# Performance work log

Measured on AMD Instinct MI355X. Metric: run time of the kernel, lower is better.

The kernel has to match this reference:

```python
import jax, jax.numpy as jnp
import numpy as np

HEADS = 12
FEATURES = 768
D_HEAD = FEATURES // HEADS
SCALE = float(np.sqrt(D_HEAD))
EPS = 1e-12
N = 2048


def setup_inputs() -> dict:
    key = jax.random.key(0)
    ks = jax.random.split(key, 5)
    init = 1.0 / np.sqrt(FEATURES)
    return {
        "x": jax.random.normal(ks[0], (N, FEATURES), dtype=jnp.float32),
        "Wq": jax.random.normal(ks[1], (FEATURES, FEATURES), dtype=jnp.float32) * init,
        "Wk": jax.random.normal(ks[2], (FEATURES, FEATURES), dtype=jnp.float32) * init,
        "Wv": jax.random.normal(ks[3], (FEATURES, FEATURES), dtype=jnp.float32) * init,
        "Wo": jax.random.normal(ks[4], (FEATURES, FEATURES), dtype=jnp.float32) * init,
        "gamma": jnp.ones((FEATURES,), dtype=jnp.float32),
        "beta": jnp.zeros((FEATURES,), dtype=jnp.float32),
    }


def reference(x, Wq, Wk, Wv, Wo, gamma, beta):
    n = x.shape[0]
    # projections (no bias); weight layout [out, in] -> x @ W.T
    q = (x @ Wq.T).reshape(n, HEADS, D_HEAD).transpose(1, 0, 2)  # [h, n, d]
    k = (x @ Wk.T).reshape(n, HEADS, D_HEAD).transpose(1, 0, 2)
    v = (x @ Wv.T).reshape(n, HEADS, D_HEAD).transpose(1, 0, 2)
    # scores [h, n, n]; original divides q@k^T by sqrt(d_head)
    att = jnp.einsum("hnd,hmd->hnm", q, k) / SCALE
    att = jax.nn.softmax(att, axis=-1)  # dropout p=0 -> identity
    out = jnp.einsum("hnm,hmd->hnd", att, v)  # [h, n, d]
    out = out.transpose(1, 0, 2).reshape(n, FEATURES)  # n (h d)
    out = out @ Wo.T
    # residual + layernorm (eps=1e-12)
    y = out + x
    mu = jnp.mean(y, axis=-1, keepdims=True)
    var = jnp.mean((y - mu) ** 2, axis=-1, keepdims=True)
    return (y - mu) / jnp.sqrt(var + EPS) * gamma + beta
```

## Files before the change

### kernel.cpp

```cpp
#include <hip/hip_runtime.h>
#include <hip/hip_bf16.h>
#include <math.h>

#define N_TOK 2048
#define FEAT  768
#define HEADS 12
#define DHEAD 64
#define SPLIT 4
#define KV_PER (N_TOK / SPLIT)

typedef __bf16 v8bf __attribute__((ext_vector_type(8)));
typedef __bf16 v4bf __attribute__((ext_vector_type(4)));
typedef float  v4f  __attribute__((ext_vector_type(4)));

#define XE ((size_t)N_TOK * FEAT)
#define WE ((size_t)FEAT * FEAT)
#define QK_LD 1536

#define SCALE_FOLD 0.18033688011112042f

__device__ __forceinline__ void gload16(const __bf16* g, __bf16* l) {
    __builtin_amdgcn_global_load_lds(
        (const __attribute__((address_space(1))) unsigned int*)g,
        (__attribute__((address_space(3))) unsigned int*)l, 16, 0, 0);
}

__global__ __launch_bounds__(256) void cvt_all(
        const float* __restrict__ x,  const float* __restrict__ Wq,
        const float* __restrict__ Wk, const float* __restrict__ Wv,
        const float* __restrict__ Wo,
        __bf16* __restrict__ xb, __bf16* __restrict__ wqkv, __bf16* __restrict__ wob) {
    size_t i = ((size_t)blockIdx.x * 256 + threadIdx.x) * 4;
    const float* src; __bf16* dst; size_t off; float scale = 1.f;
    if (i < XE)               { src = x;  dst = xb;          off = i; }
    else if (i < XE + WE)     { src = Wq; dst = wqkv;        off = i - XE; scale = SCALE_FOLD; }
    else if (i < XE + 2 * WE) { src = Wk; dst = wqkv + WE;   off = i - XE - WE; }
    else if (i < XE + 3 * WE) { src = Wv; dst = wqkv + 2*WE; off = i - XE - 2*WE; }
    else                      { src = Wo; dst = wob;         off = i - XE - 3*WE; }
    float4 v = *(const float4*)(src + off);
    v4bf o;
    o[0] = (__bf16)(v.x * scale); o[1] = (__bf16)(v.y * scale);
    o[2] = (__bf16)(v.z * scale); o[3] = (__bf16)(v.w * scale);
    *(v4bf*)(dst + off) = o;
}

__global__ __launch_bounds__(256) void gemm_qkv(
        const __bf16* __restrict__ A, const __bf16* __restrict__ B,
        __bf16* __restrict__ qk, __bf16* __restrict__ vt) {
    __shared__ __bf16 As[64][32];
    __shared__ __bf16 Bs[128][32];
    const int t    = threadIdx.x;
    const int lane = t & 63, w = t >> 6;
    const int quad = lane >> 4, l15 = lane & 15;
    const int wm = w & 1, wn = w >> 1;
    const int bm = blockIdx.y * 64, bn = blockIdx.x * 128;
    const int srow = lane >> 2, scol = (lane & 3) * 8;

    v4f acc[2][4] = {};
    for (int k0 = 0; k0 < FEAT; k0 += 32) {
        gload16(A + (size_t)(bm + w * 16 + srow) * FEAT + k0 + scol,      &As[w * 16][0]);
        gload16(B + (size_t)(bn + w * 32 + srow) * FEAT + k0 + scol,      &Bs[w * 32][0]);
        gload16(B + (size_t)(bn + w * 32 + 16 + srow) * FEAT + k0 + scol, &Bs[w * 32 + 16][0]);
        __syncthreads();
        v8bf a[2], b[4];
#pragma unroll
        for (int mi = 0; mi < 2; mi++) a[mi] = *(const v8bf*)&As[wm * 32 + mi * 16 + l15][quad * 8];
#pragma unroll
        for (int ni = 0; ni < 4; ni++) b[ni] = *(const v8bf*)&Bs[wn * 64 + ni * 16 + l15][quad * 8];
#pragma unroll
        for (int mi = 0; mi < 2; mi++)
#pragma unroll
            for (int ni = 0; ni < 4; ni++)
                acc[mi][ni] = __builtin_amdgcn_mfma_f32_16x16x32_bf16(a[mi], b[ni], acc[mi][ni], 0, 0, 0);
        __syncthreads();
    }
    if (bn < 2 * FEAT) {
#pragma unroll
        for (int mi = 0; mi < 2; mi++)
#pragma unroll
            for (int ni = 0; ni < 4; ni++) {
                int col = bn + wn * 64 + ni * 16 + l15;
#pragma unroll
                for (int r = 0; r < 4; r++) {
                    int row = bm + wm * 32 + mi * 16 + quad * 4 + r;
                    qk[(size_t)row * QK_LD + col] = (__bf16)acc[mi][ni][r];
                }
            }
    } else {
#pragma unroll
        for (int mi = 0; mi < 2; mi++)
#pragma unroll
            for (int ni = 0; ni < 4; ni++) {
                int col = bn + wn * 64 + ni * 16 + l15 - 2 * FEAT;
                int row = bm + wm * 32 + mi * 16 + quad * 4;
                v4bf pk;
#pragma unroll
                for (int r = 0; r < 4; r++) pk[r] = (__bf16)acc[mi][ni][r];
                *(v4bf*)(vt + (size_t)col * N_TOK + row) = pk;
            }
    }
}

__global__ __launch_bounds__(256, 3) void attention(
        const __bf16* __restrict__ QK, const __bf16* __restrict__ vt,
        __bf16* __restrict__ Opart, float* __restrict__ lpart) {
    __shared__ __bf16 KV[2][2][64][64];
    __shared__ __bf16 PT[4][32][64];
    const int t    = threadIdx.x;
    const int lane = t & 63, w = t >> 6;
    const int quad = lane >> 4, l15 = lane & 15;
    const int h = blockIdx.y, s = blockIdx.z;
    const int q0 = blockIdx.x * 128 + w * 32;
    const int sw = (l15 & 7) * 8;

    v8bf qf[2][2];
#pragma unroll
    for (int qt = 0; qt < 2; qt++) {
        const __bf16* qp = QK + (size_t)(q0 + qt * 16 + l15) * QK_LD + h * DHEAD + quad * 8;
        qf[qt][0] = *(const v8bf*)qp;
        qf[qt][1] = *(const v8bf*)(qp + 32);
    }
    const __bf16* kg = QK + FEAT + h * DHEAD;
    const __bf16* vg = vt + (size_t)(h * DHEAD) * N_TOK;

    v4f o_acc[4][2] = {};
    float lacc[2] = {0.f, 0.f};

    const int kvbeg = s * KV_PER;
    const int lr8 = lane >> 3;

    auto stage = [&](int b, int kv0) {
#pragma unroll
        for (int i = 0; i < 2; i++) {
            int row = w * 16 + i * 8 + lr8;
            int gs  = (lane & 7) ^ (row & 7);
            gload16(kg + (size_t)(kv0 + row) * QK_LD + gs * 8, &KV[b][0][w * 16 + i * 8][0]);
            gload16(vg + (size_t)row * N_TOK + kv0 + gs * 8,   &KV[b][1][w * 16 + i * 8][0]);
        }
    };

    auto step = [&](int b) {
        v8bf kf[4][2];
#pragma unroll
        for (int kvt = 0; kvt < 4; kvt++)
#pragma unroll
            for (int ks = 0; ks < 2; ks++)
                kf[kvt][ks] = *(const v8bf*)&KV[b][0][kvt * 16 + l15][((ks * 4 + quad) ^ (l15 & 7)) * 8];
        v4f sv[4][2];
#pragma unroll
        for (int kvt = 0; kvt < 4; kvt++)
#pragma unroll
            for (int qt = 0; qt < 2; qt++) {
                v4f a = {};
                a = __builtin_amdgcn_mfma_f32_16x16x32_bf16(kf[kvt][0], qf[qt][0], a, 0, 0, 0);
                a = __builtin_amdgcn_mfma_f32_16x16x32_bf16(kf[kvt][1], qf[qt][1], a, 0, 0, 0);
                sv[kvt][qt] = a;
            }
#pragma unroll
        for (int kvt = 0; kvt < 4; kvt++)
#pragma unroll
            for (int qt = 0; qt < 2; qt++) {
                float p0 = __builtin_amdgcn_exp2f(sv[kvt][qt][0]);
                float p1 = __builtin_amdgcn_exp2f(sv[kvt][qt][1]);
                float p2 = __builtin_amdgcn_exp2f(sv[kvt][qt][2]);
                float p3 = __builtin_amdgcn_exp2f(sv[kvt][qt][3]);
                lacc[qt] += (p0 + p1) + (p2 + p3);
                v4bf pk;
                pk[0] = (__bf16)p0; pk[1] = (__bf16)p1; pk[2] = (__bf16)p2; pk[3] = (__bf16)p3;
                *(v4bf*)&PT[w][qt * 16 + l15][(kvt * 16 + quad * 4) ^ sw] = pk;
            }
        v8bf vf[2][4];
#pragma unroll
        for (int ks = 0; ks < 2; ks++)
#pragma unroll
            for (int dt = 0; dt < 4; dt++)
                vf[ks][dt] = *(const v8bf*)&KV[b][1][dt * 16 + l15][((ks * 4 + quad) ^ (l15 & 7)) * 8];
        v8bf ptf[2][2];
#pragma unroll
        for (int ks = 0; ks < 2; ks++)
#pragma unroll
            for (int qt = 0; qt < 2; qt++)
                ptf[ks][qt] = *(const v8bf*)&PT[w][qt * 16 + l15][(ks * 32 + quad * 8) ^ sw];
#pragma unroll
        for (int dt = 0; dt < 4; dt++)
#pragma unroll
            for (int ks = 0; ks < 2; ks++)
#pragma unroll
                for (int qt = 0; qt < 2; qt++)
                    o_acc[dt][qt] = __builtin_amdgcn_mfma_f32_16x16x32_bf16(vf[ks][dt], ptf[ks][qt], o_acc[dt][qt], 0, 0, 0);
    };

    stage(0, kvbeg);
    const int TILES = KV_PER / 64;
    for (int tt = 0; tt < TILES; tt++) {
        __syncthreads();
        if (tt + 1 < TILES) stage((tt + 1) & 1, kvbeg + (tt + 1) * 64);
        step(tt & 1);
    }

    __bf16* op = Opart + (size_t)s * XE;
#pragma unroll
    for (int qt = 0; qt < 2; qt++) {
        float l = lacc[qt];
        l += __shfl_xor(l, 16); l += __shfl_xor(l, 32);
        float linv = 1.0f / l;
        int q = q0 + qt * 16 + l15;
        if (quad == 0) lpart[((size_t)s * HEADS + h) * N_TOK + q] = l;
#pragma unroll
        for (int dt = 0; dt < 4; dt++) {
            v4bf pk;
#pragma unroll
            for (int r = 0; r < 4; r++) pk[r] = (__bf16)(o_acc[dt][qt][r] * linv);
            *(v4bf*)(op + (size_t)q * FEAT + h * DHEAD + dt * 16 + quad * 4) = pk;
        }
    }
}

__global__ __launch_bounds__(256) void combine(
        const __bf16* __restrict__ Op, const float* __restrict__ lp, __bf16* __restrict__ Ob) {
    size_t i = ((size_t)blockIdx.x * 256 + threadIdx.x) * 4;
    int row = (int)(i / FEAT), col = (int)(i % FEAT), h = col >> 6;
    float ls[SPLIT], tot = 0.f;
#pragma unroll
    for (int s = 0; s < SPLIT; s++) {
        ls[s] = lp[((size_t)s * HEADS + h) * N_TOK + row];
        tot += ls[s];
    }
    float inv = 1.0f / tot;
    float a0 = 0.f, a1 = 0.f, a2 = 0.f, a3 = 0.f;
#pragma unroll
    for (int s = 0; s < SPLIT; s++) {
        v4bf p = *(const v4bf*)(Op + s * XE + i);
        float wgt = ls[s] * inv;
        a0 += wgt * (float)p[0]; a1 += wgt * (float)p[1];
        a2 += wgt * (float)p[2]; a3 += wgt * (float)p[3];
    }
    v4bf o;
    o[0] = (__bf16)a0; o[1] = (__bf16)a1; o[2] = (__bf16)a2; o[3] = (__bf16)a3;
    *(v4bf*)(Ob + i) = o;
}

__global__ __launch_bounds__(256) void gemm_out(
        const __bf16* __restrict__ Ob, const __bf16* __restrict__ Wo,
        const float* __restrict__ x, float* __restrict__ Yf) {
    __shared__ __bf16 As[64][32];
    __shared__ __bf16 Bs[128][32];
    const int t    = threadIdx.x;
    const int lane = t & 63, w = t >> 6;
    const int quad = lane >> 4, l15 = lane & 15;
    const int wm = w & 1, wn = w >> 1;
    const int bm = blockIdx.y * 64, bn = blockIdx.x * 128;
    const int srow = lane >> 2, scol = (lane & 3) * 8;

    v4f acc[2][4] = {};
    for (int k0 = 0; k0 < FEAT; k0 += 32) {
        gload16(Ob + (size_t)(bm + w * 16 + srow) * FEAT + k0 + scol,      &As[w * 16][0]);
        gload16(Wo + (size_t)(bn + w * 32 + srow) * FEAT + k0 + scol,      &Bs[w * 32][0]);
        gload16(Wo + (size_t)(bn + w * 32 + 16 + srow) * FEAT + k0 + scol, &Bs[w * 32 + 16][0]);
        __syncthreads();
        v8bf a[2], b[4];
#pragma unroll
        for (int mi = 0; mi < 2; mi++) a[mi] = *(const v8bf*)&As[wm * 32 + mi * 16 + l15][quad * 8];
#pragma unroll
        for (int ni = 0; ni < 4; ni++) b[ni] = *(const v8bf*)&Bs[wn * 64 + ni * 16 + l15][quad * 8];
#pragma unroll
        for (int mi = 0; mi < 2; mi++)
#pragma unroll
            for (int ni = 0; ni < 4; ni++)
                acc[mi][ni] = __builtin_amdgcn_mfma_f32_16x16x32_bf16(a[mi], b[ni], acc[mi][ni], 0, 0, 0);
        __syncthreads();
    }
#pragma unroll
    for (int mi = 0; mi < 2; mi++)
#pragma unroll
        for (int ni = 0; ni < 4; ni++) {
            int col = bn + wn * 64 + ni * 16 + l15;
#pragma unroll
            for (int r = 0; r < 4; r++) {
                int row = bm + wm * 32 + mi * 16 + quad * 4 + r;
                Yf[(size_t)row * FEAT + col] = acc[mi][ni][r] + x[(size_t)row * FEAT + col];
            }
        }
}

__global__ __launch_bounds__(256) void ln_kernel(
        const float* __restrict__ Y, const float* __restrict__ gamma,
        const float* __restrict__ beta, float* __restrict__ out) {
    __shared__ float sbuf[4];
    const int row = blockIdx.x, t = threadIdx.x;
    const float* y = Y + (size_t)row * FEAT;
    float v0 = y[t], v1 = y[t + 256], v2 = y[t + 512];
    float s = v0 + v1 + v2;
#pragma unroll
    for (int m = 32; m; m >>= 1) s += __shfl_xor(s, m);
    if ((t & 63) == 0) sbuf[t >> 6] = s;
    __syncthreads();
    float mean = (sbuf[0] + sbuf[1] + sbuf[2] + sbuf[3]) * (1.f / FEAT);
    __syncthreads();
    float d0 = v0 - mean, d1 = v1 - mean, d2 = v2 - mean;
    float q = d0 * d0 + d1 * d1 + d2 * d2;
#pragma unroll
    for (int m = 32; m; m >>= 1) q += __shfl_xor(q, m);
    if ((t & 63) == 0) sbuf[t >> 6] = q;
    __syncthreads();
    float var = (sbuf[0] + sbuf[1] + sbuf[2] + sbuf[3]) * (1.f / FEAT);
    float rs = rsqrtf(var + 1e-12f);
    float* o = out + (size_t)row * FEAT;
    o[t]       = d0 * rs * gamma[t]       + beta[t];
    o[t + 256] = d1 * rs * gamma[t + 256] + beta[t + 256];
    o[t + 512] = d2 * rs * gamma[t + 512] + beta[t + 512];
}

extern "C" void kernel_launch(void* const* d_in, const int* in_sizes, int n_in,
                              void* d_out, int out_size, void* d_ws, size_t ws_size,
                              hipStream_t stream) {
    const float* x     = (const float*)d_in[0];
    const float* Wq    = (const float*)d_in[1];
    const float* Wk    = (const float*)d_in[2];
    const float* Wv    = (const float*)d_in[3];
    const float* Wo    = (const float*)d_in[4];
    const float* gamma = (const float*)d_in[5];
    const float* beta  = (const float*)d_in[6];
    float* out = (float*)d_out;

    char* ws = (char*)d_ws;
    size_t off = 0;
    auto alloc = [&](size_t bytes) -> void* {
        void* p = ws + off;
        off += (bytes + 255) & ~(size_t)255;
        return p;
    };
    __bf16* xb   = (__bf16*)alloc(XE * 2);
    __bf16* wqkv = (__bf16*)alloc(3 * WE * 2);
    __bf16* wob  = (__bf16*)alloc(WE * 2);
    __bf16* qk   = (__bf16*)alloc((size_t)N_TOK * QK_LD * 2);
    __bf16* vtb  = (__bf16*)alloc((size_t)FEAT * N_TOK * 2);
    __bf16* Op   = (__bf16*)alloc(SPLIT * XE * 2);
    float*  lp   = (float*)alloc(SPLIT * HEADS * N_TOK * 4);
    __bf16* Ob   = vtb;
    float*  Yf   = (float*)ws;

    cvt_all<<<(int)((XE + 4 * WE) / 4 / 256), 256, 0, stream>>>(x, Wq, Wk, Wv, Wo, xb, wqkv, wob);

    gemm_qkv<<<dim3((QK_LD + FEAT) / 128, N_TOK / 64), 256, 0, stream>>>(xb, wqkv, qk, vtb);

    attention<<<dim3(N_TOK / 128, HEADS, SPLIT), 256, 0, stream>>>(qk, vtb, Op, lp);

    combine<<<(int)(XE / 4 / 256), 256, 0, stream>>>(Op, lp, Ob);

    gemm_out<<<dim3(FEAT / 128, N_TOK / 64), 256, 0, stream>>>(Ob, wob, x, Yf);

    ln_kernel<<<N_TOK, 256, 0, stream>>>(Yf, gamma, beta, out);
}
```

Baseline: 138.7 us.

## Widen QKV GEMM k-tile with swizzled LDS and split attention step into halves

The QKV projection GEMM now stages 64-wide k slices per iteration with an XOR-swizzled LDS layout. This halves the number of barrier pairs and is meant to avoid bank conflicts. The attention inner step is split into two 32-key halves that compute scores, exponentiate, write P to a smaller LDS buffer and immediately run the PV MFMAs. That cuts live registers and LDS so launch bounds can request 4 blocks per CU instead of 3. The risk is more LDS round-trips per tile and possible register spilling under the tighter occupancy bound.

New measurement: 135.9 us. 1.02x faster.

```diff
diff --git a/kernel.cpp b/kernel.cpp
--- a/kernel.cpp
+++ b/kernel.cpp
@@ -47,31 +47,39 @@
 __global__ __launch_bounds__(256) void gemm_qkv(
         const __bf16* __restrict__ A, const __bf16* __restrict__ B,
         __bf16* __restrict__ qk, __bf16* __restrict__ vt) {
-    __shared__ __bf16 As[64][32];
-    __shared__ __bf16 Bs[128][32];
+    __shared__ __bf16 As[64][64];
+    __shared__ __bf16 Bs[128][64];
     const int t    = threadIdx.x;
     const int lane = t & 63, w = t >> 6;
     const int quad = lane >> 4, l15 = lane & 15;
     const int wm = w & 1, wn = w >> 1;
     const int bm = blockIdx.y * 64, bn = blockIdx.x * 128;
-    const int srow = lane >> 2, scol = (lane & 3) * 8;
+    const int lr8 = lane >> 3;
+    const int gs  = ((lane & 7) ^ lr8) * 8;
 
     v4f acc[2][4] = {};
-    for (int k0 = 0; k0 < FEAT; k0 += 32) {
-        gload16(A + (size_t)(bm + w * 16 + srow) * FEAT + k0 + scol,      &As[w * 16][0]);
-        gload16(B + (size_t)(bn + w * 32 + srow) * FEAT + k0 + scol,      &Bs[w * 32][0]);
-        gload16(B + (size_t)(bn + w * 32 + 16 + srow) * FEAT + k0 + scol, &Bs[w * 32 + 16][0]);
-        __syncthreads();
-        v8bf a[2], b[4];
-#pragma unroll
-        for (int mi = 0; mi < 2; mi++) a[mi] = *(const v8bf*)&As[wm * 32 + mi * 16 + l15][quad * 8];
-#pragma unroll
-        for (int ni = 0; ni < 4; ni++) b[ni] = *(const v8bf*)&Bs[wn * 64 + ni * 16 + l15][quad * 8];
-#pragma unroll
-        for (int mi = 0; mi < 2; mi++)
-#pragma unroll
-            for (int ni = 0; ni < 4; ni++)
-                acc[mi][ni] = __builtin_amdgcn_mfma_f32_16x16x32_bf16(a[mi], b[ni], acc[mi][ni], 0, 0, 0);
+    for (int k0 = 0; k0 < FEAT; k0 += 64) {
+        gload16(A + (size_t)(bm + w * 16 +      lr8) * FEAT + k0 + gs, &As[w * 16][0]);
+        gload16(A + (size_t)(bm + w * 16 + 8 +  lr8) * FEAT + k0 + gs, &As[w * 16 + 8][0]);
+        gload16(B + (size_t)(bn + w * 32 +      lr8) * FEAT + k0 + gs, &Bs[w * 32][0]);
+        gload16(B + (size_t)(bn + w * 32 + 8 +  lr8) * FEAT + k0 + gs, &Bs[w * 32 + 8][0]);
+        gload16(B + (size_t)(bn + w * 32 + 16 + lr8) * FEAT + k0 + gs, &Bs[w * 32 + 16][0]);
+        gload16(B + (size_t)(bn + w * 32 + 24 + lr8) * FEAT + k0 + gs, &Bs[w * 32 + 24][0]);
+        __syncthreads();
+#pragma unroll
+        for (int kk = 0; kk < 2; kk++) {
+            const int fo = ((kk * 4 + quad) ^ (l15 & 7)) * 8;
+            v8bf a[2], b[4];
+#pragma unroll
+            for (int mi = 0; mi < 2; mi++) a[mi] = *(const v8bf*)&As[wm * 32 + mi * 16 + l15][fo];
+#pragma unroll
+            for (int ni = 0; ni < 4; ni++) b[ni] = *(const v8bf*)&Bs[wn * 64 + ni * 16 + l15][fo];
+#pragma unroll
+            for (int mi = 0; mi < 2; mi++)
+#pragma unroll
+                for (int ni = 0; ni < 4; ni++)
+                    acc[mi][ni] = __builtin_amdgcn_mfma_f32_16x16x32_bf16(a[mi], b[ni], acc[mi][ni], 0, 0, 0);
+        }
         __syncthreads();
     }
     if (bn < 2 * FEAT) {
@@ -101,17 +109,17 @@
     }
 }
 
-__global__ __launch_bounds__(256, 3) void attention(
+__global__ __launch_bounds__(256, 4) void attention(
         const __bf16* __restrict__ QK, const __bf16* __restrict__ vt,
         __bf16* __restrict__ Opart, float* __restrict__ lpart) {
     __shared__ __bf16 KV[2][2][64][64];
-    __shared__ __bf16 PT[4][32][64];
+    __shared__ __bf16 PT[4][32][32];
     const int t    = threadIdx.x;
     const int lane = t & 63, w = t >> 6;
     const int quad = lane >> 4, l15 = lane & 15;
     const int h = blockIdx.y, s = blockIdx.z;
     const int q0 = blockIdx.x * 128 + w * 32;
-    const int sw = (l15 & 7) * 8;
+    const int sw3 = l15 & 3;
 
     v8bf qf[2][2];
 #pragma unroll
@@ -133,61 +141,49 @@
 #pragma unroll
         for (int i = 0; i < 2; i++) {
             int row = w * 16 + i * 8 + lr8;
-            int gs  = (lane & 7) ^ (row & 7);
-            gload16(kg + (size_t)(kv0 + row) * QK_LD + gs * 8, &KV[b][0][w * 16 + i * 8][0]);
-            gload16(vg + (size_t)row * N_TOK + kv0 + gs * 8,   &KV[b][1][w * 16 + i * 8][0]);
+            int gsk = (lane & 7) ^ (row & 7);
+            gload16(kg + (size_t)(kv0 + row) * QK_LD + gsk * 8, &KV[b][0][w * 16 + i * 8][0]);
+            gload16(vg + (size_t)row * N_TOK + kv0 + gsk * 8,   &KV[b][1][w * 16 + i * 8][0]);
         }
     };
 
     auto step = [&](int b) {
-        v8bf kf[4][2];
-#pragma unroll
-        for (int kvt = 0; kvt < 4; kvt++)
-#pragma unroll
-            for (int ks = 0; ks < 2; ks++)
-                kf[kvt][ks] = *(const v8bf*)&KV[b][0][kvt * 16 + l15][((ks * 4 + quad) ^ (l15 & 7)) * 8];
-        v4f sv[4][2];
-#pragma unroll
-        for (int kvt = 0; kvt < 4; kvt++)
-#pragma unroll
-            for (int qt = 0; qt < 2; qt++) {
-                v4f a = {};
-                a = __builtin_amdgcn_mfma_f32_16x16x32_bf16(kf[kvt][0], qf[qt][0], a, 0, 0, 0);
-                a = __builtin_amdgcn_mfma_f32_16x16x32_bf16(kf[kvt][1], qf[qt][1], a, 0, 0, 0);
-                sv[kvt][qt] = a;
+#pragma unroll
+        for (int half = 0; half < 2; half++) {
+#pragma unroll
+            for (int kk = 0; kk < 2; kk++) {
+                int kvt = half * 2 + kk;
+                v8bf kf0 = *(const v8bf*)&KV[b][0][kvt * 16 + l15][((0 + quad) ^ (l15 & 7)) * 8];
+                v8bf kf1 = *(const v8bf*)&KV[b][0][kvt * 16 + l15][((4 + quad) ^ (l15 & 7)) * 8];
+                const int wcol = ((kk * 2 + (quad >> 1)) ^ sw3) * 8 + (quad & 1) * 4;
+#pragma unroll
+                for (int qt = 0; qt < 2; qt++) {
+                    v4f a = {};
+                    a = __builtin_amdgcn_mfma_f32_16x16x32_bf16(kf0, qf[qt][0], a, 0, 0, 0);
+                    a = __builtin_amdgcn_mfma_f32_16x16x32_bf16(kf1, qf[qt][1], a, 0, 0, 0);
+                    float p0 = __builtin_amdgcn_exp2f(a[0]);
+                    float p1 = __builtin_amdgcn_exp2f(a[1]);
+                    float p2 = __builtin_amdgcn_exp2f(a[2]);
+                    float p3 = __builtin_amdgcn_exp2f(a[3]);
+                    lacc[qt] += (p0 + p1) + (p2 + p3);
+                    v4bf pk;
+                    pk[0] = (__bf16)p0; pk[1] = (__bf16)p1; pk[2] = (__bf16)p2; pk[3] = (__bf16)p3;
+                    *(v4bf*)&PT[w][qt * 16 + l15][wcol] = pk;
+                }
             }
-#pragma unroll
-        for (int kvt = 0; kvt < 4; kvt++)
-#pragma unroll
-            for (int qt = 0; qt < 2; qt++) {
-                float p0 = __builtin_amdgcn_exp2f(sv[kvt][qt][0]);
-                float p1 = __builtin_amdgcn_exp2f(sv[kvt][qt][1]);
-                float p2 = __builtin_amdgcn_exp2f(sv[kvt][qt][2]);
-                float p3 = __builtin_amdgcn_exp2f(sv[kvt][qt][3]);
-                lacc[qt] += (p0 + p1) + (p2 + p3);
-                v4bf pk;
-                pk[0] = (__bf16)p0; pk[1] = (__bf16)p1; pk[2] = (__bf16)p2; pk[3] = (__bf16)p3;
-                *(v4bf*)&PT[w][qt * 16 + l15][(kvt * 16 + quad * 4) ^ sw] = pk;
-            }
-        v8bf vf[2][4];
-#pragma unroll
-        for (int ks = 0; ks < 2; ks++)
+            v8bf vf[4], ptf[2];
 #pragma unroll
             for (int dt = 0; dt < 4; dt++)
-                vf[ks][dt] = *(const v8bf*)&KV[b][1][dt * 16 + l15][((ks * 4 + quad) ^ (l15 & 7)) * 8];
-        v8bf ptf[2][2];
-#pragma unroll
-        for (int ks = 0; ks < 2; ks++)
+                vf[dt] = *(const v8bf*)&KV[b][1][dt * 16 + l15][((half * 4 + quad) ^ (l15 & 7)) * 8];
 #pragma unroll
             for (int qt = 0; qt < 2; qt++)
-                ptf[ks][qt] = *(const v8bf*)&PT[w][qt * 16 + l15][(ks * 32 + quad * 8) ^ sw];
-#pragma unroll
-        for (int dt = 0; dt < 4; dt++)
-#pragma unroll
-            for (int ks = 0; ks < 2; ks++)
+                ptf[qt] = *(const v8bf*)&PT[w][qt * 16 + l15][(quad ^ sw3) * 8];
+#pragma unroll
+            for (int dt = 0; dt < 4; dt++)
 #pragma unroll
                 for (int qt = 0; qt < 2; qt++)
-                    o_acc[dt][qt] = __builtin_amdgcn_mfma_f32_16x16x32_bf16(vf[ks][dt], ptf[ks][qt], o_acc[dt][qt], 0, 0, 0);
+                    o_acc[dt][qt] = __builtin_amdgcn_mfma_f32_16x16x32_bf16(vf[dt], ptf[qt], o_acc[dt][qt], 0, 0, 0);
+        }
     };
 
     stage(0, kvbeg);
```
